# Optimization experiments

Hardware: AMD Instinct MI355X
Metric: run time of the kernel (lower is better)

The kernel has to match this reference:

```python
import jax, jax.numpy as jnp
import numpy as np

N, F_IN, HID, PROJ, K = 10000, 256, 128, 64, 50
E, HEADS = 320000, 8


def _p(key, shape, scale=0.05):
    return jax.random.normal(key, shape, dtype=jnp.float32) * scale


def setup_inputs() -> dict:
    key = jax.random.key(0)
    ks = jax.random.split(key, 20)
    x = jax.random.normal(ks[0], (N, F_IN), dtype=jnp.float32)
    edge_index = jax.random.randint(ks[1], (2, E), 0, N, dtype=jnp.int64)
    return {
        "x": x,
        "edge_index": edge_index,
        "lin1_w": _p(ks[2], (HID, F_IN)), "lin1_b": _p(ks[3], (HID,)),
        "gat1_w": _p(ks[4], (HEADS * HID, F_IN)),
        "gat1_att_src": _p(ks[5], (HEADS, HID)), "gat1_att_dst": _p(ks[6], (HEADS, HID)),
        "gat1_b": _p(ks[7], (HEADS * HID,)),
        "gat2_w": _p(ks[8], (HID, HEADS * HID)),
        "gat2_att_src": _p(ks[9], (1, HID)), "gat2_att_dst": _p(ks[10], (1, HID)),
        "gat2_b": _p(ks[11], (HID,)),
        "proj_w": _p(ks[12], (PROJ, 2 * HID)), "proj_b": _p(ks[13], (PROJ,)),
        "ln_g": jnp.ones((2 * HID,), jnp.float32), "ln_b": jnp.zeros((2 * HID,), jnp.float32),
        "lin_w": _p(ks[14], (64, 4 * HID)), "lin_b": _p(ks[15], (64,)),
    }


def gat_conv(x, src, dst, W, a_src, a_dst, b, concat):
    # PyG GATConv, add_self_loops=False, eval mode (no attention dropout).
    H, C = a_src.shape
    n = x.shape[0]
    h = (x @ W.T).reshape(n, H, C)                      # [N,H,C]
    al_src = jnp.einsum('nhc,hc->nh', h, a_src)          # [N,H]
    al_dst = jnp.einsum('nhc,hc->nh', h, a_dst)
    e = jax.nn.leaky_relu(al_src[src] + al_dst[dst], 0.2)  # [E,H]
    emax = jax.ops.segment_max(e, dst, num_segments=n)
    ex = jnp.exp(e - emax[dst])
    denom = jax.ops.segment_sum(ex, dst, num_segments=n) + 1e-16
    alpha = ex / denom[dst]                              # [E,H]
    out = jax.ops.segment_sum(h[src] * alpha[:, :, None], dst, num_segments=n)  # [N,H,C]
    if concat:
        return out.reshape(n, H * C) + b
    return out.mean(axis=1) + b


def knn_mean(g_score, final, k):
    # dense pairwise sq-distance + top-k (replaces CPU KDTree loop), gather-mean
    sq = jnp.sum(g_score * g_score, axis=1)
    neg_d2 = 2.0 * (g_score @ g_score.T) - sq[:, None] - sq[None, :]
    idx = jax.lax.top_k(jax.lax.stop_gradient(neg_d2), k)[1]  # [N,k]
    return jnp.mean(final[idx], axis=1)                        # [N,2h]


def reference(x, edge_index, lin1_w, lin1_b, gat1_w, gat1_att_src, gat1_att_dst,
              gat1_b, gat2_w, gat2_att_src, gat2_att_dst, gat2_b, proj_w, proj_b,
              ln_g, ln_b, lin_w, lin_b):
    src, dst = edge_index[0], edge_index[1]
    x1 = jax.nn.relu(x @ lin1_w.T + lin1_b)                              # MLP branch
    xg = jax.nn.relu(gat_conv(x, src, dst, gat1_w, gat1_att_src, gat1_att_dst, gat1_b, True))
    x2 = gat_conv(xg, src, dst, gat2_w, gat2_att_src, gat2_att_dst, gat2_b, False)
    final = jnp.concatenate([x1, x2], axis=1)                            # [N,2h]
    g_score = final @ proj_w.T + proj_b                                  # [N,proj]
    sim = knn_mean(g_score, final, K)                                    # [N,2h]
    mu = sim.mean(axis=-1, keepdims=True)
    var = sim.var(axis=-1, keepdims=True)
    sim = (sim - mu) * jax.lax.rsqrt(var + 1e-5) * ln_g + ln_b           # LayerNorm
    out = jnp.concatenate([final, sim], axis=1) @ lin_w.T + lin_b        # [N,64]
    return out
```

## Files before the change

kernel.cpp:

```cpp
#include <hip/hip_runtime.h>

#define FIN 256
#define KNN 50
#define JB  2000
#define CAP 128

static __device__ __forceinline__ float lrelu02(float v){ return v > 0.f ? v : 0.2f*v; }
static __device__ __forceinline__ unsigned fkey(float v){
  unsigned u = __float_as_uint(v);
  return (u & 0x80000000u) ? ~u : (u | 0x80000000u);
}

__global__ __launch_bounds__(256) void k_zero_int(int* p, int n){
  int i = blockIdx.x*256 + threadIdx.x; if (i<n) p[i]=0;
}
__global__ __launch_bounds__(256) void k_count_deg(const int* __restrict__ dstv, int* deg, int E){
  int i = blockIdx.x*256 + threadIdx.x; if (i<E) atomicAdd(&deg[dstv[i]], 1);
}
__global__ __launch_bounds__(256) void k_scan(const int* __restrict__ deg, int* offs, int* cursor, int n){
  __shared__ int buf[256]; __shared__ int carry;
  int t = threadIdx.x;
  if (t==0) carry = 0;
  __syncthreads();
  for (int base=0; base<n; base+=256){
    int v = (base+t<n)? deg[base+t] : 0;
    buf[t]=v; __syncthreads();
    for (int off=1; off<256; off<<=1){
      int add = (t>=off)? buf[t-off] : 0;
      __syncthreads();
      buf[t]+=add; __syncthreads();
    }
    int excl = buf[t]-v+carry;
    if (base+t<n){ offs[base+t]=excl; cursor[base+t]=excl; }
    __syncthreads();
    if (t==0) carry += buf[255];
    __syncthreads();
  }
}
__global__ __launch_bounds__(256) void k_fill_csr(const int* __restrict__ dstv, int* cursor, int* csr, int E){
  int i = blockIdx.x*256 + threadIdx.x;
  if (i<E){ int p=atomicAdd(&cursor[dstv[i]],1); csr[p]=i; }
}
__global__ __launch_bounds__(64) void k_sort_csr_wave(int* csr, const int* __restrict__ offs, const int* __restrict__ deg, int n){
  int node = blockIdx.x; if (node>=n) return;
  int t = threadIdx.x;
  int st = offs[node], d = deg[node];
  __shared__ int buf[256];
  if (d > 256){
    if (t==0){
      for (int a=1;a<d;++a){ int v=csr[st+a]; int b=a-1;
        while (b>=0 && csr[st+b]>v){ csr[st+b+1]=csr[st+b]; --b; }
        csr[st+b+1]=v; }
    }
    return;
  }
  for (int q=t;q<d;q+=64) buf[q]=csr[st+q];
  __syncthreads();
  for (int it=0; it<d; ++it){
    int ph = it & 1;
    for (int pidx=t; 2*pidx+ph+1 < d; pidx+=64){
      int a = 2*pidx+ph;
      int va=buf[a], vb=buf[a+1];
      if (va > vb){ buf[a]=vb; buf[a+1]=va; }
    }
    __syncthreads();
  }
  for (int q=t;q<d;q+=64) csr[st+q]=buf[q];
}

__global__ __launch_bounds__(256) void k_fold(
  const float* __restrict__ W, const float* __restrict__ as8, const float* __restrict__ ad8,
  float* __restrict__ Wf)
{
  int o = blockIdx.x;
  int t = threadIdx.x;
  int h = o & 7;
  const float* av = (o<8) ? (as8 + h*128) : (ad8 + h*128);
  const float* wp = W + (size_t)h*128*256 + t;
  float acc = 0.f;
  #pragma unroll 4
  for (int c=0;c<128;++c) acc += av[c] * wp[(size_t)c*256];
  Wf[o*256+t] = acc;
}

__global__ __launch_bounds__(256) void gemm_bt(
    const float* __restrict__ A, int lda,
    const float* __restrict__ W, int ldw,
    const float* __restrict__ bias,
    float* __restrict__ C, int ldc, int coff,
    int M, int Kdim, int O, int relu,
    int az, int wz, int cz, int bz)
{
  A += (size_t)blockIdx.z * az;
  W += (size_t)blockIdx.z * wz;
  if (bias) bias += (size_t)blockIdx.z * bz;
  coff += blockIdx.z * cz;
  __shared__ float As[32][68];
  __shared__ float Ws[32][68];
  int t  = threadIdx.x;
  int n0 = blockIdx.y * 64;
  int o0 = blockIdx.x * 64;
  int tx = t & 15, ty = t >> 4;
  float acc[4][4] = {};
  int kgrp = t & 7;
  int row  = t >> 3;
  for (int k0 = 0; k0 < Kdim; k0 += 32) {
    #pragma unroll
    for (int p = 0; p < 2; ++p) {
      int r = row + 32*p;
      int n = n0 + r;
      float4 v = make_float4(0.f,0.f,0.f,0.f);
      if (n < M) v = *(const float4*)(A + (size_t)n*lda + k0 + 4*kgrp);
      As[4*kgrp+0][r] = v.x; As[4*kgrp+1][r] = v.y;
      As[4*kgrp+2][r] = v.z; As[4*kgrp+3][r] = v.w;
      int o = o0 + r;
      float4 w = make_float4(0.f,0.f,0.f,0.f);
      if (o < O) w = *(const float4*)(W + (size_t)o*ldw + k0 + 4*kgrp);
      Ws[4*kgrp+0][r] = w.x; Ws[4*kgrp+1][r] = w.y;
      Ws[4*kgrp+2][r] = w.z; Ws[4*kgrp+3][r] = w.w;
    }
    __syncthreads();
    #pragma unroll 8
    for (int kk = 0; kk < 32; ++kk) {
      float4 a = *(const float4*)&As[kk][ty*4];
      float4 w = *(const float4*)&Ws[kk][tx*4];
      float av[4] = {a.x,a.y,a.z,a.w};
      float wv[4] = {w.x,w.y,w.z,w.w};
      #pragma unroll
      for (int i=0;i<4;++i)
        #pragma unroll
        for (int j=0;j<4;++j) acc[i][j] += av[i]*wv[j];
    }
    __syncthreads();
  }
  #pragma unroll
  for (int i=0;i<4;++i) {
    int n = n0 + ty*4 + i;
    if (n >= M) continue;
    #pragma unroll
    for (int j=0;j<4;++j) {
      int o = o0 + tx*4 + j;
      if (o >= O) continue;
      float v = acc[i][j] + (bias ? bias[o] : 0.f);
      if (relu) v = fmaxf(v, 0.f);
      C[(size_t)n*ldc + coff + o] = v;
    }
  }
}

__global__ __launch_bounds__(256) void gemm128(
    const float* __restrict__ A, int lda,
    const float* __restrict__ W, int ldw,
    const float* __restrict__ bias,
    float* __restrict__ C, int ldc, int coff,
    int M, int Kdim, int relu,
    int az, int wz, int cz, int bz)
{
  A += (size_t)blockIdx.z * az;
  W += (size_t)blockIdx.z * wz;
  const float* bp = bias + (size_t)blockIdx.z * bz;
  int ccol = coff + blockIdx.z * cz;
  __shared__ float As[32][132];
  __shared__ float Ws[32][132];
  int t = threadIdx.x;
  int n0 = blockIdx.y * 128;
  int kg = t & 7, rb = t >> 3;
  int tx = t & 15, ty = t >> 4;
  float acc[2][2][4][4] = {};
  for (int k0 = 0; k0 < Kdim; k0 += 32) {
    __syncthreads();
    #pragma unroll
    for (int p = 0; p < 4; ++p) {
      int r = rb + 32*p;
      int n = n0 + r;
      float4 v = make_float4(0.f,0.f,0.f,0.f);
      if (n < M) v = *(const float4*)(A + (size_t)n*lda + k0 + 4*kg);
      As[4*kg+0][r]=v.x; As[4*kg+1][r]=v.y; As[4*kg+2][r]=v.z; As[4*kg+3][r]=v.w;
      float4 w = *(const float4*)(W + (size_t)r*ldw + k0 + 4*kg);
      Ws[4*kg+0][r]=w.x; Ws[4*kg+1][r]=w.y; Ws[4*kg+2][r]=w.z; Ws[4*kg+3][r]=w.w;
    }
    __syncthreads();
    #pragma unroll 8
    for (int kk = 0; kk < 32; ++kk) {
      float4 A0 = *(const float4*)&As[kk][ty*4];
      float4 A1 = *(const float4*)&As[kk][64+ty*4];
      float4 B0 = *(const float4*)&Ws[kk][tx*4];
      float4 B1 = *(const float4*)&Ws[kk][64+tx*4];
      float av[2][4] = {{A0.x,A0.y,A0.z,A0.w},{A1.x,A1.y,A1.z,A1.w}};
      float bv[2][4] = {{B0.x,B0.y,B0.z,B0.w},{B1.x,B1.y,B1.z,B1.w}};
      #pragma unroll
      for (int pi=0;pi<2;++pi)
        #pragma unroll
        for (int pj=0;pj<2;++pj)
          #pragma unroll
          for (int i=0;i<4;++i)
            #pragma unroll
            for (int j=0;j<4;++j)
              acc[pi][pj][i][j] += av[pi][i]*bv[pj][j];
    }
  }
  #pragma unroll
  for (int pi=0;pi<2;++pi)
    #pragma unroll
    for (int i=0;i<4;++i) {
      int n = n0 + pi*64 + ty*4 + i;
      if (n >= M) continue;
      #pragma unroll
      for (int pj=0;pj<2;++pj)
        #pragma unroll
        for (int j=0;j<4;++j) {
          int o = pj*64 + tx*4 + j;
          float v = acc[pi][pj][i][j] + bp[o];
          if (relu) v = fmaxf(v, 0.f);
          C[(size_t)n*ldc + ccol + o] = v;
        }
    }
}

__global__ __launch_bounds__(256) void att_logits(
    const float* __restrict__ hbuf, const float* __restrict__ asrc,
    const float* __restrict__ adst, float* __restrict__ als, float* __restrict__ ald,
    int H, int M)
{
  int gidx = blockIdx.x*256 + threadIdx.x;
  if (gidx >= M*H) return;
  int n = gidx / H, h = gidx % H;
  const float* hp = hbuf + (size_t)n*H*128 + (size_t)h*128;
  const float* as = asrc + h*128;
  const float* ad = adst + h*128;
  float s1=0.f, s2=0.f;
  for (int c=0;c<128;++c){ float v=hp[c]; s1 += v*as[c]; s2 += v*ad[c]; }
  als[gidx]=s1; ald[gidx]=s2;
}

template<int NH>
__global__ __launch_bounds__(256) void gat1_agg_x(
    const float* __restrict__ x, const float* __restrict__ al1,
    const int* __restrict__ csr, const int* __restrict__ offs, const int* __restrict__ deg,
    const int* __restrict__ srcv,
    float* __restrict__ agg, int h0, int M)
{
  const int n = blockIdx.x, t = threadIdx.x;
  const int d = deg[n], st = offs[n];
  const int lane = t & 63, w = t >> 6;
  __shared__ float sh_ald[NH];
  __shared__ float wpart[4*NH];
  __shared__ float emax_s[NH], den_s[NH];
  __shared__ int   s_lds[128];
  __shared__ float alpha_lds[128*NH];
  if (t < NH) sh_ald[t] = al1[(size_t)n*16 + 8 + h0 + t];
  __syncthreads();
  float lm[NH];
  #pragma unroll
  for (int h=0;h<NH;++h) lm[h] = -__builtin_inff();
  for (int q=t; q<d; q+=256) {
    int s = srcv[csr[st+q]];
    float av[NH];
    float4 a0 = *(const float4*)(al1 + (size_t)s*16 + h0);
    av[0]=a0.x; av[1]=a0.y; av[2]=a0.z; av[3]=a0.w;
    if constexpr (NH==8){
      float4 a1 = *(const float4*)(al1 + (size_t)s*16 + h0 + 4);
      av[4]=a1.x; av[5]=a1.y; av[6]=a1.z; av[7]=a1.w;
    }
    #pragma unroll
    for (int h=0;h<NH;++h) lm[h] = fmaxf(lm[h], lrelu02(av[h] + sh_ald[h]));
  }
  #pragma unroll
  for (int h=0;h<NH;++h){
    float v = lm[h];
    for (int off=32;off>0;off>>=1) v = fmaxf(v, __shfl_down(v, off, 64));
    if (lane==0) wpart[w*NH+h] = v;
  }
  __syncthreads();
  if (t < NH)
    emax_s[t] = fmaxf(fmaxf(wpart[t], wpart[NH+t]), fmaxf(wpart[2*NH+t], wpart[3*NH+t]));
  __syncthreads();
  float ls[NH];
  #pragma unroll
  for (int h=0;h<NH;++h) ls[h]=0.f;
  for (int q=t; q<d; q+=256) {
    int s = srcv[csr[st+q]];
    float av[NH];
    float4 a0 = *(const float4*)(al1 + (size_t)s*16 + h0);
    av[0]=a0.x; av[1]=a0.y; av[2]=a0.z; av[3]=a0.w;
    if constexpr (NH==8){
      float4 a1 = *(const float4*)(al1 + (size_t)s*16 + h0 + 4);
      av[4]=a1.x; av[5]=a1.y; av[6]=a1.z; av[7]=a1.w;
    }
    #pragma unroll
    for (int h=0;h<NH;++h) ls[h] += expf(lrelu02(av[h] + sh_ald[h]) - emax_s[h]);
  }
  #pragma unroll
  for (int h=0;h<NH;++h){
    float v = ls[h];
    for (int off=32;off>0;off>>=1) v += __shfl_down(v, off, 64);
    if (lane==0) wpart[w*NH+h] = v;
  }
  __syncthreads();
  if (t < NH)
    den_s[t] = wpart[t] + wpart[NH+t] + wpart[2*NH+t] + wpart[3*NH+t] + 1e-16f;
  float acc[NH];
  #pragma unroll
  for (int h=0;h<NH;++h) acc[h]=0.f;
  for (int c0=0; c0<d; c0+=128) {
    int cl = min(128, d-c0);
    __syncthreads();
    for (int q=t; q<cl; q+=256) s_lds[q] = srcv[csr[st+c0+q]];
    __syncthreads();
    for (int idx=t; idx<cl*NH; idx+=256) {
      int q = idx / NH, h = idx % NH;
      float als = al1[(size_t)s_lds[q]*16 + h0 + h];
      float v = lrelu02(als + sh_ald[h]);
      alpha_lds[q*NH+h] = expf(v - emax_s[h]) / den_s[h];
    }
    __syncthreads();
    for (int q=0; q<cl; ++q) {
      float xv = x[(size_t)s_lds[q]*FIN + t];
      #pragma unroll
      for (int h=0;h<NH;++h) acc[h] += alpha_lds[q*NH+h] * xv;
    }
  }
  #pragma unroll
  for (int h=0;h<NH;++h) agg[(size_t)n*(NH*256) + h*256 + t] = acc[h];
}

__global__ __launch_bounds__(256) void gat2_agg_wave(
  const float* __restrict__ h2, const float* __restrict__ als, const float* __restrict__ ald,
  const int* __restrict__ csr, const int* __restrict__ offs, const int* __restrict__ deg,
  const int* __restrict__ srcv, const float* __restrict__ bias,
  float* __restrict__ cat, int M)
{
  int wid = blockIdx.x*4 + (threadIdx.x>>6);
  int lane = threadIdx.x & 63;
  if (wid >= M) return;
  int d = deg[wid], st = offs[wid];
  float aldn = ald[wid];
  float lm = -__builtin_inff();
  for (int q=lane;q<d;q+=64){ int s=srcv[csr[st+q]]; lm = fmaxf(lm, lrelu02(als[s]+aldn)); }
  #pragma unroll
  for (int m=1;m<64;m<<=1) lm = fmaxf(lm, __shfl_xor(lm, m, 64));
  float ls = 0.f;
  for (int q=lane;q<d;q+=64){ int s=srcv[csr[st+q]]; ls += expf(lrelu02(als[s]+aldn)-lm); }
  #pragma unroll
  for (int m=1;m<64;m<<=1) ls += __shfl_xor(ls, m, 64);
  float den = ls + 1e-16f;
  float a0=0.f, a1=0.f;
  for (int q=0;q<d;++q){
    int s = srcv[csr[st+q]];
    float alpha = expf(lrelu02(als[s]+aldn)-lm)/den;
    float2 hv = *(const float2*)(h2 + (size_t)s*128 + lane*2);
    a0 += alpha*hv.x; a1 += alpha*hv.y;
  }
  a0 += bias[lane*2]; a1 += bias[lane*2+1];
  *(float2*)(cat + (size_t)wid*512 + 128 + lane*2) = make_float2(a0,a1);
}

__global__ __launch_bounds__(256) void k_sq(const float* __restrict__ g, float* sq, int n){
  int i = blockIdx.x*256+threadIdx.x;
  if (i<n){ const float* p=g+(size_t)i*64; float s=0.f; for(int c=0;c<64;++c) s+=p[c]*p[c]; sq[i]=s; }
}
__global__ __launch_bounds__(256) void k_init_topk(unsigned int* tk, int* ti, int n){
  int i = blockIdx.x*256+threadIdx.x;
  if (i<n){ tk[i]=0u; ti[i]=0x7fffffff; }
}

__global__ __launch_bounds__(256) void gram128(
    const float* __restrict__ G, const float* __restrict__ sqv,
    const unsigned* __restrict__ kth,
    float* __restrict__ slab, int* __restrict__ cnt,
    unsigned* __restrict__ ck, int* __restrict__ ci,
    int j0, int M, int use_filter)
{
  __shared__ float Gi[64][132];
  __shared__ float Gj[64][132];
  int t = threadIdx.x;
  int i0  = blockIdx.y * 128;
  int jt0 = blockIdx.x * 128;
  int kg = t & 15, rb = t >> 4;
  #pragma unroll
  for (int p=0;p<8;++p){
    int r = rb + 16*p;
    int i = i0 + r;
    float4 v = (i<M) ? *(const float4*)(G + (size_t)i*64 + 4*kg) : make_float4(0,0,0,0);
    Gi[4*kg+0][r]=v.x; Gi[4*kg+1][r]=v.y; Gi[4*kg+2][r]=v.z; Gi[4*kg+3][r]=v.w;
    int j = j0 + jt0 + r;
    float4 w = (j<M) ? *(const float4*)(G + (size_t)j*64 + 4*kg) : make_float4(0,0,0,0);
    Gj[4*kg+0][r]=w.x; Gj[4*kg+1][r]=w.y; Gj[4*kg+2][r]=w.z; Gj[4*kg+3][r]=w.w;
  }
  __syncthreads();
  int tx = t & 15, ty = t >> 4;
  float acc[2][2][4][4] = {};
  #pragma unroll 8
  for (int k=0;k<64;++k){
    float4 A0 = *(const float4*)&Gi[k][ty*4];
    float4 A1 = *(const float4*)&Gi[k][64+ty*4];
    float4 B0 = *(const float4*)&Gj[k][tx*4];
    float4 B1 = *(const float4*)&Gj[k][64+tx*4];
    float av[2][4] = {{A0.x,A0.y,A0.z,A0.w},{A1.x,A1.y,A1.z,A1.w}};
    float bv[2][4] = {{B0.x,B0.y,B0.z,B0.w},{B1.x,B1.y,B1.z,B1.w}};
    #pragma unroll
    for (int pi=0;pi<2;++pi)
      #pragma unroll
      for (int pj=0;pj<2;++pj)
        #pragma unroll
        for (int i=0;i<4;++i)
          #pragma unroll
          for (int j=0;j<4;++j)
            acc[pi][pj][i][j] += av[pi][i]*bv[pj][j];
  }
  #pragma unroll
  for (int pi=0;pi<2;++pi)
    #pragma unroll
    for (int i=0;i<4;++i){
      int ii = i0 + pi*64 + ty*4 + i;
      if (ii >= M) continue;
      float sqi = sqv[ii];
      #pragma unroll
      for (int pj=0;pj<2;++pj){
        int jl0 = jt0 + pj*64 + tx*4;
        if (jl0 >= JB) continue;
        float4 v4;
        v4.x = 2.f*acc[pi][pj][i][0] - sqi - sqv[j0+jl0+0];
        v4.y = 2.f*acc[pi][pj][i][1] - sqi - sqv[j0+jl0+1];
        v4.z = 2.f*acc[pi][pj][i][2] - sqi - sqv[j0+jl0+2];
        v4.w = 2.f*acc[pi][pj][i][3] - sqi - sqv[j0+jl0+3];
        *(float4*)(slab + (size_t)ii*JB + jl0) = v4;
        if (use_filter){
          unsigned kt = kth[ii];
          float vv[4] = {v4.x, v4.y, v4.z, v4.w};
          #pragma unroll
          for (int j=0;j<4;++j){
            unsigned key = fkey(vv[j]);
            if (key > kt){
              int pos = atomicAdd(&cnt[ii], 1);
              if (pos < CAP){ ck[(size_t)ii*CAP+pos] = key; ci[(size_t)ii*CAP+pos] = j0+jl0+j; }
            }
          }
        }
      }
    }
}

__global__ __launch_bounds__(256) void topk_update(
    const float* __restrict__ slab, int j0, int jcount,
    const unsigned* __restrict__ ck, const int* __restrict__ ci, const int* __restrict__ cnt,
    unsigned* __restrict__ tkk, int* __restrict__ tki, unsigned* __restrict__ kth,
    int M, int force_radix)
{
  int i = blockIdx.x, t = threadIdx.x;
  int c = force_radix ? (CAP+1) : cnt[i];
  if (c <= CAP) {
    __shared__ unsigned skey[256];
    __shared__ int sidx[256];
    unsigned k = 0u; int id = 0x7fffffff;
    if (t < KNN){ k = tkk[(size_t)i*KNN+t]; id = tki[(size_t)i*KNN+t]; }
    else if (t-KNN < c){ k = ck[(size_t)i*CAP + (t-KNN)]; id = ci[(size_t)i*CAP + (t-KNN)]; }
    skey[t] = k; sidx[t] = id;
    for (int size=2; size<=256; size<<=1){
      for (int stride=size>>1; stride>0; stride>>=1){
        __syncthreads();
        int p = t ^ stride;
        if (p > t){
          unsigned k1=skey[t], k2=skey[p]; int i1=sidx[t], i2=sidx[p];
          bool b21 = (k2>k1) || (k2==k1 && i2<i1);
          bool b12 = (k1>k2) || (k1==k2 && i1<i2);
          bool desc = ((t & size) == 0);
          if (desc ? b21 : b12){
            skey[t]=k2; skey[p]=k1; sidx[t]=i2; sidx[p]=i1;
          }
        }
      }
    }
    __syncthreads();
    if (t < KNN){ tkk[(size_t)i*KNN+t] = skey[t]; tki[(size_t)i*KNN+t] = sidx[t]; }
    if (t == 0) kth[i] = skey[KNN-1];
  } else {
    __shared__ unsigned keys[JB + KNN];
    __shared__ int hist[256];
    __shared__ int red2[256];
    __shared__ int oldidx[KNN];
    __shared__ int outidx[KNN];
    __shared__ unsigned outkey[KNN];
    __shared__ int b_star, cnt2;
    for (int p=t; p<jcount; p+=256) keys[p] = fkey(slab[(size_t)i*JB + p]);
    for (int p=jcount+t; p<JB; p+=256) keys[p] = 0u;
    if (t < KNN){ keys[JB+t] = tkk[(size_t)i*KNN+t]; oldidx[t] = tki[(size_t)i*KNN+t]; }
    if (t == 0) cnt2 = 0;
    __syncthreads();
    const int total = JB + KNN;
    unsigned prefix = 0, pmask = 0;
    int need = KNN;
    #pragma unroll
    for (int pass=0; pass<4; ++pass) {
      int shift = 24 - 8*pass;
      hist[t] = 0; __syncthreads();
      for (int p=t; p<total; p+=256) {
        unsigned k = keys[p];
        if ((k & pmask) == prefix) atomicAdd(&hist[(k>>shift)&255], 1);
      }
      __syncthreads();
      for (int off=1; off<256; off<<=1) {
        int v = (t+off<256) ? hist[t+off] : 0;
        __syncthreads();
        hist[t] += v;
        __syncthreads();
      }
      if (hist[t] >= need && (t==255 || hist[t+1] < need)) b_star = t;
      __syncthreads();
      int b = b_star;
      need -= (b < 255) ? hist[b+1] : 0;
      prefix |= ((unsigned)b) << shift;
      pmask  |= 0xFFu << shift;
      __syncthreads();
    }
    for (int p=t; p<total; p+=256) {
      unsigned k = keys[p];
      if (k > prefix) {
        int pos = atomicAdd(&cnt2, 1);
        outidx[pos] = (p < JB) ? (j0 + p) : oldidx[p-JB];
        outkey[pos] = k;
      }
    }
    __syncthreads();
    int base = cnt2;
    int last = -1;
    for (int it=0; it<need; ++it) {
      int best = 0x7fffffff;
      for (int p=t; p<total; p+=256) {
        if (keys[p] == prefix) {
          int idx = (p < JB) ? (j0 + p) : oldidx[p-JB];
          if (idx > last && idx < best) best = idx;
        }
      }
      red2[t] = best; __syncthreads();
      for (int s=128;s>0;s>>=1){ if (t<s) red2[t] = min(red2[t], red2[t+s]); __syncthreads(); }
      if (t==0) { outidx[base+it] = red2[0]; outkey[base+it] = prefix; }
      last = red2[0];
      __syncthreads();
    }
    if (t < KNN){ tkk[(size_t)i*KNN+t] = outkey[t]; tki[(size_t)i*KNN+t] = outidx[t]; }
    if (t == 0) kth[i] = prefix;
  }
}

__global__ __launch_bounds__(256) void knn_mean_ln(
    float* __restrict__ cat, const int* __restrict__ topi,
    const float* __restrict__ g, const float* __restrict__ b, int M)
{
  int i = blockIdx.x; int t = threadIdx.x;
  __shared__ int idx[KNN];
  __shared__ float red[256];
  if (t<KNN) idx[t]=topi[(size_t)i*KNN+t];
  __syncthreads();
  float acc=0.f;
  for (int r=0;r<KNN;++r) acc += cat[(size_t)idx[r]*512 + t];
  float xval = acc * (1.f/KNN);
  red[t]=xval; __syncthreads();
  for (int s=128;s>0;s>>=1){ if(t<s) red[t]+=red[t+s]; __syncthreads(); }
  float mu = red[0]*(1.f/256.f); __syncthreads();
  float d = xval-mu;
  red[t]=d*d; __syncthreads();
  for (int s=128;s>0;s>>=1){ if(t<s) red[t]+=red[t+s]; __syncthreads(); }
  float var = red[0]*(1.f/256.f);
  float y = d * rsqrtf(var+1e-5f) * g[t] + b[t];
  cat[(size_t)i*512 + 256 + t] = y;
}

extern "C" void kernel_launch(void* const* d_in, const int* in_sizes, int n_in,
                              void* d_out, int out_size, void* d_ws, size_t ws_size,
                              hipStream_t stream)
{
  const float* x      = (const float*)d_in[0];
  const int*   ei     = (const int*)  d_in[1];
  const float* lin1_w = (const float*)d_in[2];
  const float* lin1_b = (const float*)d_in[3];
  const float* gat1_w = (const float*)d_in[4];
  const float* g1_as  = (const float*)d_in[5];
  const float* g1_ad  = (const float*)d_in[6];
  const float* gat1_b = (const float*)d_in[7];
  const float* gat2_w = (const float*)d_in[8];
  const float* g2_as  = (const float*)d_in[9];
  const float* g2_ad  = (const float*)d_in[10];
  const float* gat2_b = (const float*)d_in[11];
  const float* proj_w = (const float*)d_in[12];
  const float* proj_b = (const float*)d_in[13];
  const float* ln_g   = (const float*)d_in[14];
  const float* ln_b   = (const float*)d_in[15];
  const float* lin_w  = (const float*)d_in[16];
  const float* lin_b  = (const float*)d_in[17];
  float* outp = (float*)d_out;

  const int N = in_sizes[0]/FIN;
  const int E = in_sizes[1]/2;
  const int* srcv = ei;
  const int* dstv = ei + E;

  size_t needFull = sizeof(float)*((size_t)N*(2048+1024+512+16+128+1+1+64+1+KNN+KNN+1+1+1+1+1+2*CAP) + E + 4096);
  bool full = ws_size >= needFull;
  size_t aggF = full ? (size_t)N*2048 : (size_t)N*1024;

  float* ws = (float*)d_ws;
  size_t f = 0;
  float* agg  = ws + f; f += aggF;
  float* xg   = ws + f; f += (size_t)N*1024;
  float* slab = agg;
  float* cat  = ws + f; f += (size_t)N*512;
  float* al1  = ws + f; f += (size_t)N*16;
  float* h2   = ws + f; f += (size_t)N*128;
  float* al2s = ws + f; f += (size_t)N;
  float* al2d = ws + f; f += (size_t)N;
  float* gsc  = ws + f; f += (size_t)N*64;
  float* sqv  = ws + f; f += (size_t)N;
  unsigned* tkk = (unsigned*)(ws + f); f += (size_t)N*KNN;
  int* tki    = (int*)(ws + f); f += (size_t)N*KNN;
  int* deg    = (int*)(ws + f); f += (size_t)N;
  int* offs   = (int*)(ws + f); f += (size_t)N;
  int* cursor = (int*)(ws + f); f += (size_t)N;
  unsigned* kth = (unsigned*)(ws + f); f += (size_t)N;
  int* ccnt   = (int*)(ws + f); f += (size_t)N;
  unsigned* ck = (unsigned*)(ws + f); f += (size_t)N*CAP;
  int* ci     = (int*)(ws + f); f += (size_t)N*CAP;
  int* csr    = (int*)(ws + f); f += (size_t)E;
  float* Wf   = ws + f; f += 4096;
  (void)n_in; (void)out_size;

  dim3 b256(256);
  int gy = (N+63)/64;
  int gy128 = (N+127)/128;

  k_zero_int<<<(N+255)/256, b256, 0, stream>>>(deg, N);
  k_count_deg<<<(E+255)/256, b256, 0, stream>>>(dstv, deg, E);
  k_scan<<<1, b256, 0, stream>>>(deg, offs, cursor, N);
  k_fill_csr<<<(E+255)/256, b256, 0, stream>>>(dstv, cursor, csr, E);
  k_sort_csr_wave<<<N, dim3(64), 0, stream>>>(csr, offs, deg, N);

  k_fold<<<16, b256, 0, stream>>>(gat1_w, g1_as, g1_ad, Wf);
  gemm_bt<<<dim3(1,gy,1), b256, 0, stream>>>(x,FIN, Wf,FIN, nullptr, al1,16,0, N,FIN,16, 0, 0,0,0,0);

  gemm_bt<<<dim3(2,gy,1), b256, 0, stream>>>(x,FIN, lin1_w,FIN, lin1_b, cat,512,0, N,FIN,128, 1, 0,0,0,0);

  if (full) {
    gat1_agg_x<8><<<N, b256, 0, stream>>>(x, al1, csr, offs, deg, srcv, agg, 0, N);
    gemm128<<<dim3(1,gy128,8), b256, 0, stream>>>(agg,2048, gat1_w,FIN, gat1_b, xg,1024,0,
                                                  N,FIN, 1, 256, 128*256, 128, 128);
  } else {
    for (int h0=0; h0<8; h0+=4) {
      gat1_agg_x<4><<<N, b256, 0, stream>>>(x, al1, csr, offs, deg, srcv, agg, h0, N);
      gemm128<<<dim3(1,gy128,4), b256, 0, stream>>>(agg,1024, gat1_w + (size_t)h0*128*256,FIN,
                                                    gat1_b + h0*128, xg,1024, h0*128,
                                                    N,FIN, 1, 256, 128*256, 128, 128);
    }
  }

  gemm_bt<<<dim3(2,gy,1), b256, 0, stream>>>(xg,1024, gat2_w,1024, nullptr, h2,128,0, N,1024,128, 0, 0,0,0,0);
  att_logits<<<(N+255)/256, b256, 0, stream>>>(h2, g2_as, g2_ad, al2s, al2d, 1, N);
  gat2_agg_wave<<<(N+3)/4, b256, 0, stream>>>(h2, al2s, al2d, csr, offs, deg, srcv, gat2_b, cat, N);

  gemm_bt<<<dim3(1,gy,1), b256, 0, stream>>>(cat,512, proj_w,256, proj_b, gsc,64,0, N,256,64, 0, 0,0,0,0);
  k_sq<<<(N+255)/256, b256, 0, stream>>>(gsc, sqv, N);
  k_init_topk<<<(N*KNN+255)/256, b256, 0, stream>>>(tkk, tki, N*KNN);
  k_zero_int<<<(N+255)/256, b256, 0, stream>>>((int*)kth, N);
  for (int j0=0; j0<N; j0+=JB){
    int jc = (N - j0 < JB) ? (N - j0) : JB;
    int first = (j0 == 0);
    k_zero_int<<<(N+255)/256, b256, 0, stream>>>(ccnt, N);
    gram128<<<dim3((JB+127)/128, gy128), b256, 0, stream>>>(gsc, sqv, kth, slab, ccnt, ck, ci, j0, N, !first);
    topk_update<<<N, b256, 0, stream>>>(slab, j0, jc, ck, ci, ccnt, tkk, tki, kth, N, first);
  }
  knn_mean_ln<<<N, b256, 0, stream>>>(cat, tki, ln_g, ln_b, N);
  gemm_bt<<<dim3(1,gy,1), b256, 0, stream>>>(cat,512, lin_w,512, lin_b, outp,64,0, N,512,64, 0, 0,0,0,0);
}
```

Measured before the change: 1.449 ms.

## Skip slab writes after first KNN chunk and recompute distances on overflow

After the first column chunk, the gram kernel no longer writes the full N×2000 distance slab. It only emits filtered candidates above the current kth key. Rows whose candidate list overflows recompute their distances directly from the projection vectors inside the top-k kernel. The gram tile staging is also changed to two half-K passes with an XOR-swizzled float4 shared-memory layout to reduce bank conflicts, and the first-chunk radix path is split into its own kernel. The goal is to remove most slab write and read traffic and one zeroing launch, at the cost of extra recompute on overflow rows and a smaller shared-memory footprint per K pass.

```diff
diff --git a/kernel.cpp b/kernel.cpp
--- a/kernel.cpp
+++ b/kernel.cpp
@@ -364,49 +364,65 @@
   if (i<n){ tk[i]=0u; ti[i]=0x7fffffff; }
 }
 
-__global__ __launch_bounds__(256) void gram128(
+template<int MODE>
+__global__ __launch_bounds__(256) void gram128v2(
     const float* __restrict__ G, const float* __restrict__ sqv,
     const unsigned* __restrict__ kth,
     float* __restrict__ slab, int* __restrict__ cnt,
     unsigned* __restrict__ ck, int* __restrict__ ci,
-    int j0, int M, int use_filter)
-{
-  __shared__ float Gi[64][132];
-  __shared__ float Gj[64][132];
+    int j0, int M)
+{
+  __shared__ float4 GiS[32*32];
+  __shared__ float4 GjS[32*32];
+  float* Gif = (float*)GiS;
+  float* Gjf = (float*)GjS;
   int t = threadIdx.x;
   int i0  = blockIdx.y * 128;
   int jt0 = blockIdx.x * 128;
-  int kg = t & 15, rb = t >> 4;
-  #pragma unroll
-  for (int p=0;p<8;++p){
-    int r = rb + 16*p;
-    int i = i0 + r;
-    float4 v = (i<M) ? *(const float4*)(G + (size_t)i*64 + 4*kg) : make_float4(0,0,0,0);
-    Gi[4*kg+0][r]=v.x; Gi[4*kg+1][r]=v.y; Gi[4*kg+2][r]=v.z; Gi[4*kg+3][r]=v.w;
-    int j = j0 + jt0 + r;
-    float4 w = (j<M) ? *(const float4*)(G + (size_t)j*64 + 4*kg) : make_float4(0,0,0,0);
-    Gj[4*kg+0][r]=w.x; Gj[4*kg+1][r]=w.y; Gj[4*kg+2][r]=w.z; Gj[4*kg+3][r]=w.w;
-  }
-  __syncthreads();
   int tx = t & 15, ty = t >> 4;
+  int kg = t & 7, rg = t >> 3;
   float acc[2][2][4][4] = {};
-  #pragma unroll 8
-  for (int k=0;k<64;++k){
-    float4 A0 = *(const float4*)&Gi[k][ty*4];
-    float4 A1 = *(const float4*)&Gi[k][64+ty*4];
-    float4 B0 = *(const float4*)&Gj[k][tx*4];
-    float4 B1 = *(const float4*)&Gj[k][64+tx*4];
-    float av[2][4] = {{A0.x,A0.y,A0.z,A0.w},{A1.x,A1.y,A1.z,A1.w}};
-    float bv[2][4] = {{B0.x,B0.y,B0.z,B0.w},{B1.x,B1.y,B1.z,B1.w}};
-    #pragma unroll
-    for (int pi=0;pi<2;++pi)
+  #pragma unroll
+  for (int h=0; h<2; ++h) {
+    if (h) __syncthreads();
+    #pragma unroll
+    for (int rr=0; rr<4; ++rr) {
+      int r = rg + 32*rr;
+      int slotw = (r>>2) ^ kg;
+      int gi = i0 + r;
+      float4 v = (gi<M) ? *(const float4*)(G + (size_t)gi*64 + h*32 + 4*kg) : make_float4(0,0,0,0);
+      Gif[((4*kg+0)*32 + slotw)*4 + (r&3)] = v.x;
+      Gif[((4*kg+1)*32 + slotw)*4 + (r&3)] = v.y;
+      Gif[((4*kg+2)*32 + slotw)*4 + (r&3)] = v.z;
+      Gif[((4*kg+3)*32 + slotw)*4 + (r&3)] = v.w;
+      int gj = j0 + jt0 + r;
+      float4 w = (gj<M) ? *(const float4*)(G + (size_t)gj*64 + h*32 + 4*kg) : make_float4(0,0,0,0);
+      Gjf[((4*kg+0)*32 + slotw)*4 + (r&3)] = w.x;
+      Gjf[((4*kg+1)*32 + slotw)*4 + (r&3)] = w.y;
+      Gjf[((4*kg+2)*32 + slotw)*4 + (r&3)] = w.z;
+      Gjf[((4*kg+3)*32 + slotw)*4 + (r&3)] = w.w;
+    }
+    __syncthreads();
+    #pragma unroll 8
+    for (int k=0; k<32; ++k) {
+      int kc3 = (k>>2)&7;
+      int sa = ty ^ kc3, sb = tx ^ kc3;
+      float4 A0 = GiS[k*32 + sa];
+      float4 A1 = GiS[k*32 + 16 + sa];
+      float4 B0 = GjS[k*32 + sb];
+      float4 B1 = GjS[k*32 + 16 + sb];
+      float av[2][4] = {{A0.x,A0.y,A0.z,A0.w},{A1.x,A1.y,A1.z,A1.w}};
+      float bv[2][4] = {{B0.x,B0.y,B0.z,B0.w},{B1.x,B1.y,B1.z,B1.w}};
       #pragma unroll
-      for (int pj=0;pj<2;++pj)
+      for (int pi=0;pi<2;++pi)
         #pragma unroll
-        for (int i=0;i<4;++i)
+        for (int pj=0;pj<2;++pj)
           #pragma unroll
-          for (int j=0;j<4;++j)
-            acc[pi][pj][i][j] += av[pi][i]*bv[pj][j];
+          for (int i=0;i<4;++i)
+            #pragma unroll
+            for (int j=0;j<4;++j)
+              acc[pi][pj][i][j] += av[pi][i]*bv[pj][j];
+    }
   }
   #pragma unroll
   for (int pi=0;pi<2;++pi)
@@ -424,8 +440,9 @@
         v4.y = 2.f*acc[pi][pj][i][1] - sqi - sqv[j0+jl0+1];
         v4.z = 2.f*acc[pi][pj][i][2] - sqi - sqv[j0+jl0+2];
         v4.w = 2.f*acc[pi][pj][i][3] - sqi - sqv[j0+jl0+3];
-        *(float4*)(slab + (size_t)ii*JB + jl0) = v4;
-        if (use_filter){
+        if (MODE == 0) {
+          *(float4*)(slab + (size_t)ii*JB + jl0) = v4;
+        } else {
           unsigned kt = kth[ii];
           float vv[4] = {v4.x, v4.y, v4.z, v4.w};
           #pragma unroll
@@ -441,14 +458,86 @@
     }
 }
 
-__global__ __launch_bounds__(256) void topk_update(
+__global__ __launch_bounds__(256) void topk_radix(
     const float* __restrict__ slab, int j0, int jcount,
+    unsigned* __restrict__ tkk, int* __restrict__ tki, unsigned* __restrict__ kth, int M)
+{
+  __shared__ unsigned keys[JB + KNN];
+  __shared__ int hist[256];
+  __shared__ int red2[256];
+  __shared__ int oldidx[KNN];
+  __shared__ int outidx[KNN];
+  __shared__ unsigned outkey[KNN];
+  __shared__ int b_star, cnt2;
+  int i = blockIdx.x, t = threadIdx.x;
+  for (int p=t; p<jcount; p+=256) keys[p] = fkey(slab[(size_t)i*JB + p]);
+  for (int p=jcount+t; p<JB; p+=256) keys[p] = 0u;
+  if (t < KNN){ keys[JB+t] = tkk[(size_t)i*KNN+t]; oldidx[t] = tki[(size_t)i*KNN+t]; }
+  if (t == 0) cnt2 = 0;
+  __syncthreads();
+  const int total = JB + KNN;
+  unsigned prefix = 0, pmask = 0;
+  int need = KNN;
+  #pragma unroll
+  for (int pass=0; pass<4; ++pass) {
+    int shift = 24 - 8*pass;
+    hist[t] = 0; __syncthreads();
+    for (int p=t; p<total; p+=256) {
+      unsigned k = keys[p];
+      if ((k & pmask) == prefix) atomicAdd(&hist[(k>>shift)&255], 1);
+    }
+    __syncthreads();
+    for (int off=1; off<256; off<<=1) {
+      int v = (t+off<256) ? hist[t+off] : 0;
+      __syncthreads();
+      hist[t] += v;
+      __syncthreads();
+    }
+    if (hist[t] >= need && (t==255 || hist[t+1] < need)) b_star = t;
+    __syncthreads();
+    int b = b_star;
+    need -= (b < 255) ? hist[b+1] : 0;
+    prefix |= ((unsigned)b) << shift;
+    pmask  |= 0xFFu << shift;
+    __syncthreads();
+  }
+  for (int p=t; p<total; p+=256) {
+    unsigned k = keys[p];
+    if (k > prefix) {
+      int pos = atomicAdd(&cnt2, 1);
+      outidx[pos] = (p < JB) ? (j0 + p) : oldidx[p-JB];
+      outkey[pos] = k;
+    }
+  }
+  __syncthreads();
+  int base = cnt2;
+  int last = -1;
+  for (int it=0; it<need; ++it) {
+    int best = 0x7fffffff;
+    for (int p=t; p<total; p+=256) {
+      if (keys[p] == prefix) {
+        int idx = (p < JB) ? (j0 + p) : oldidx[p-JB];
+        if (idx > last && idx < best) best = idx;
+      }
+    }
+    red2[t] = best; __syncthreads();
+    for (int s=128;s>0;s>>=1){ if (t<s) red2[t] = min(red2[t], red2[t+s]); __syncthreads(); }
+    if (t==0) { outidx[base+it] = red2[0]; outkey[base+it] = prefix; }
+    last = red2[0];
+    __syncthreads();
+  }
+  if (t < KNN){ tkk[(size_t)i*KNN+t] = outkey[t]; tki[(size_t)i*KNN+t] = outidx[t]; }
+  if (t == 0) kth[i] = prefix;
+}
+
+__global__ __launch_bounds__(256) void topk_fast(
+    const float* __restrict__ G, const float* __restrict__ sqv,
+    int j0, int jcount,
     const unsigned* __restrict__ ck, const int* __restrict__ ci, const int* __restrict__ cnt,
-    unsigned* __restrict__ tkk, int* __restrict__ tki, unsigned* __restrict__ kth,
-    int M, int force_radix)
+    unsigned* __restrict__ tkk, int* __restrict__ tki, unsigned* __restrict__ kth, int M)
 {
   int i = blockIdx.x, t = threadIdx.x;
-  int c = force_radix ? (CAP+1) : cnt[i];
+  int c = cnt[i];
   if (c <= CAP) {
     __shared__ unsigned skey[256];
     __shared__ int sidx[256];
@@ -475,6 +564,7 @@
     if (t < KNN){ tkk[(size_t)i*KNN+t] = skey[t]; tki[(size_t)i*KNN+t] = sidx[t]; }
     if (t == 0) kth[i] = skey[KNN-1];
   } else {
+    __shared__ float gvec[64];
     __shared__ unsigned keys[JB + KNN];
     __shared__ int hist[256];
     __shared__ int red2[256];
@@ -482,10 +572,25 @@
     __shared__ int outidx[KNN];
     __shared__ unsigned outkey[KNN];
     __shared__ int b_star, cnt2;
-    for (int p=t; p<jcount; p+=256) keys[p] = fkey(slab[(size_t)i*JB + p]);
+    if (t < 64) gvec[t] = G[(size_t)i*64 + t];
+    if (t == 0) cnt2 = 0;
+    __syncthreads();
+    float sqi = sqv[i];
+    for (int p=t; p<jcount; p+=256){
+      const float4* gj4 = (const float4*)(G + (size_t)(j0+p)*64);
+      float acc = 0.f;
+      #pragma unroll 4
+      for (int q=0;q<16;++q){
+        float4 w = gj4[q];
+        acc += gvec[4*q+0]*w.x;
+        acc += gvec[4*q+1]*w.y;
+        acc += gvec[4*q+2]*w.z;
+        acc += gvec[4*q+3]*w.w;
+      }
+      keys[p] = fkey(2.f*acc - sqi - sqv[j0+p]);
+    }
     for (int p=jcount+t; p<JB; p+=256) keys[p] = 0u;
     if (t < KNN){ keys[JB+t] = tkk[(size_t)i*KNN+t]; oldidx[t] = tki[(size_t)i*KNN+t]; }
-    if (t == 0) cnt2 = 0;
     __syncthreads();
     const int total = JB + KNN;
     unsigned prefix = 0, pmask = 0;
@@ -659,13 +764,16 @@
   gemm_bt<<<dim3(1,gy,1), b256, 0, stream>>>(cat,512, proj_w,256, proj_b, gsc,64,0, N,256,64, 0, 0,0,0,0);
   k_sq<<<(N+255)/256, b256, 0, stream>>>(gsc, sqv, N);
   k_init_topk<<<(N*KNN+255)/256, b256, 0, stream>>>(tkk, tki, N*KNN);
-  k_zero_int<<<(N+255)/256, b256, 0, stream>>>((int*)kth, N);
   for (int j0=0; j0<N; j0+=JB){
     int jc = (N - j0 < JB) ? (N - j0) : JB;
-    int first = (j0 == 0);
-    k_zero_int<<<(N+255)/256, b256, 0, stream>>>(ccnt, N);
-    gram128<<<dim3((JB+127)/128, gy128), b256, 0, stream>>>(gsc, sqv, kth, slab, ccnt, ck, ci, j0, N, !first);
-    topk_update<<<N, b256, 0, stream>>>(slab, j0, jc, ck, ci, ccnt, tkk, tki, kth, N, first);
+    if (j0 == 0) {
+      gram128v2<0><<<dim3((JB+127)/128, gy128), b256, 0, stream>>>(gsc, sqv, kth, slab, ccnt, ck, ci, j0, N);
+      topk_radix<<<N, b256, 0, stream>>>(slab, j0, jc, tkk, tki, kth, N);
+    } else {
+      k_zero_int<<<(N+255)/256, b256, 0, stream>>>(ccnt, N);
+      gram128v2<1><<<dim3((JB+127)/128, gy128), b256, 0, stream>>>(gsc, sqv, kth, slab, ccnt, ck, ci, j0, N);
+      topk_fast<<<N, b256, 0, stream>>>(gsc, sqv, j0, jc, ck, ci, ccnt, tkk, tki, kth, N);
+    }
   }
   knn_mean_ln<<<N, b256, 0, stream>>>(cat, tki, ln_g, ln_b, N);
   gemm_bt<<<dim3(1,gy,1), b256, 0, stream>>>(cat,512, lin_w,512, lin_b, outp,64,0, N,512,64, 0, 0,0,0,0);
```

Result: faster. 1.402 ms (-3.2%).
